# Performance work log

Hardware: AMD Instinct MI355X
Metric: run time of the kernel (lower is better)

Reference implementation:

```python
import jax, jax.numpy as jnp
import numpy as np

D_MODEL = 1024
NUM_HEADS = 16
HEAD_DIM = D_MODEL // NUM_HEADS
BATCH, SEQ = 2, 2048


def setup_inputs() -> dict:
    key = jax.random.key(0)
    ks = jax.random.split(key, 11)
    s = 1.0 / np.sqrt(D_MODEL)
    inp = {
        "query": jax.random.normal(ks[0], (BATCH, SEQ, D_MODEL), jnp.float32),
        "key": jax.random.normal(ks[1], (BATCH, SEQ, D_MODEL), jnp.float32),
        "value": jax.random.normal(ks[2], (BATCH, SEQ, D_MODEL), jnp.float32),
        "q_w": jax.random.uniform(ks[3], (D_MODEL, D_MODEL), jnp.float32, -s, s),
        "q_b": jax.random.uniform(ks[4], (D_MODEL,), jnp.float32, -s, s),
        "k_w": jax.random.uniform(ks[5], (D_MODEL, D_MODEL), jnp.float32, -s, s),
        "k_b": jax.random.uniform(ks[6], (D_MODEL,), jnp.float32, -s, s),
        "v_w": jax.random.uniform(ks[7], (D_MODEL, D_MODEL), jnp.float32, -s, s),
        "v_b": jax.random.uniform(ks[8], (D_MODEL,), jnp.float32, -s, s),
        "o_w": jax.random.uniform(ks[9], (D_MODEL, D_MODEL), jnp.float32, -s, s),
        "o_b": jax.random.uniform(ks[10], (D_MODEL,), jnp.float32, -s, s),
    }
    return inp


def reference(query, key, value, q_w, q_b, k_w, k_b, v_w, v_b, o_w, o_b):
    B = query.shape[0]
    # linear projections (torch Linear: x @ W^T + b)
    q = query @ q_w.T + q_b
    k = key @ k_w.T + k_b
    v = value @ v_w.T + v_b
    # split heads: [B, S, D] -> [B, H, S, Hd]
    def split(x):
        return x.reshape(B, -1, NUM_HEADS, HEAD_DIM).transpose(0, 2, 1, 3)
    q, k, v = split(q), split(k), split(v)
    scores = jnp.einsum("bhqd,bhkd->bhqk", q, k) / np.sqrt(HEAD_DIM).astype(np.float32)
    attn = jax.nn.softmax(scores, axis=-1)
    out = jnp.einsum("bhqk,bhkd->bhqd", attn, v)  # [B,H,S,Hd]
    merged = out.transpose(0, 2, 1, 3).reshape(B, -1, D_MODEL)
    return merged @ o_w.T + o_b
```

## Files before the change

### kernel.cpp

```cpp
#include <hip/hip_runtime.h>
#include <hip/hip_bf16.h>

typedef unsigned short u16;
typedef unsigned int u32;
typedef __attribute__((ext_vector_type(8))) short short8;
typedef __attribute__((ext_vector_type(4))) short s16x4;
typedef __attribute__((ext_vector_type(4))) float f32x4;
typedef __attribute__((ext_vector_type(4))) u32 u32v4;

__device__ __forceinline__ u16 f2bf(float f) {
    u32 u = __float_as_uint(f);
    return (u16)((u + 0x7FFFu + ((u >> 16) & 1u)) >> 16);
}
__device__ __forceinline__ u32 pack2bf(float a, float b) {
    __hip_bfloat162 h = __float22bfloat162_rn(float2{a, b});
    return *reinterpret_cast<u32*>(&h);
}
__device__ __forceinline__ float exp2hw(float x) {
    float r;
    asm("v_exp_f32 %0, %1" : "=v"(r) : "v"(x));
    return r;
}

__device__ __forceinline__ void gload16(const void* g, void* s) {
    __builtin_amdgcn_global_load_lds(
        (const __attribute__((address_space(1))) void*)g,
        (__attribute__((address_space(3))) void*)s, 16, 0, 0);
}

__global__ __launch_bounds__(256) void cast_all_kernel(
    const float* __restrict__ s0, const float* __restrict__ s1, const float* __restrict__ s2,
    const float* __restrict__ s3, const float* __restrict__ s4, const float* __restrict__ s5,
    const float* __restrict__ s6,
    u16* __restrict__ d0, u16* __restrict__ d1, u16* __restrict__ d2,
    u16* __restrict__ d3, u16* __restrict__ d4, u16* __restrict__ d5,
    u16* __restrict__ d6, int nBig, int nSmall)
{
    const int y = blockIdx.y;
    const float* s = y == 0 ? s0 : (y == 1 ? s1 : (y == 2 ? s2 : (y == 3 ? s3 : (y == 4 ? s4 : (y == 5 ? s5 : s6)))));
    u16* d = y == 0 ? d0 : (y == 1 ? d1 : (y == 2 ? d2 : (y == 3 ? d3 : (y == 4 ? d4 : (y == 5 ? d5 : d6)))));
    const int n = (y < 3) ? nBig : nSmall;
    int i = (blockIdx.x * 256 + threadIdx.x) * 4;
    const int stride = gridDim.x * 256 * 4;
    for (; i < n; i += stride) {
        float4 v = *(const float4*)(s + i);
        uint2 t;
        t.x = pack2bf(v.x, v.y);
        t.y = pack2bf(v.z, v.w);
        *(uint2*)(d + i) = t;
    }
}

__global__ __launch_bounds__(256) void qkv_gemm(
    const u16* __restrict__ Xq, const u16* __restrict__ Xk, const u16* __restrict__ Xv,
    const u16* __restrict__ Wqkv,
    const float* __restrict__ qb, const float* __restrict__ kb, const float* __restrict__ vb,
    u16* __restrict__ Qo, u16* __restrict__ Ko, u16* __restrict__ Vo)
{
    constexpr int K = 1024;
    __shared__ __align__(16) u16 Asm[2][4096];
    __shared__ __align__(16) u16 Bsm[2][4096];

    const int tid = threadIdx.x;
    const int wid = tid >> 6;
    const int lane = tid & 63;
    const int r15 = lane & 15, g = lane >> 4;
    const int flat = blockIdx.x;
    const int wgid = (flat & 7) * 96 + (flat >> 3);
    const int m0 = (wgid / 24) * 128;
    const int nAll = (wgid % 24) * 128;
    const int z = nAll >> 10;
    const u16* A = z == 0 ? Xq : (z == 1 ? Xk : Xv);
    const int wr = wid >> 1, wc = wid & 1;

    f32x4 acc[4][4];
#pragma unroll
    for (int i = 0; i < 4; ++i)
#pragma unroll
        for (int j = 0; j < 4; ++j) acc[i][j] = (f32x4){0.f, 0.f, 0.f, 0.f};

    const int idx0 = tid, idx1 = tid + 256;
    const size_t aoff0 = (size_t)(m0 + (idx0 >> 2)) * K + (idx0 & 3) * 8;
    const size_t aoff1 = (size_t)(m0 + (idx1 >> 2)) * K + (idx1 & 3) * 8;
    const size_t boff0 = (size_t)(nAll + (idx0 >> 2)) * K + (idx0 & 3) * 8;
    const size_t boff1 = (size_t)(nAll + (idx1 >> 2)) * K + (idx1 & 3) * 8;
    const u16* abase = &Asm[0][0] + (wr * 64 + r15) * 32 + g * 8;
    const u16* bbase = &Bsm[0][0] + (wc * 64 + r15) * 32 + g * 8;

    gload16(A + aoff0, &Asm[0][wid * 512]);
    gload16(A + aoff1, &Asm[0][2048 + wid * 512]);
    gload16(Wqkv + boff0, &Bsm[0][wid * 512]);
    gload16(Wqkv + boff1, &Bsm[0][2048 + wid * 512]);
    __syncthreads();

#pragma unroll 2
    for (int t = 0; t < 32; ++t) {
        const int buf = t & 1;
        if (t < 31) {
            const int kt = (t + 1) * 32;
            gload16(A + aoff0 + kt, &Asm[buf ^ 1][wid * 512]);
            gload16(A + aoff1 + kt, &Asm[buf ^ 1][2048 + wid * 512]);
            gload16(Wqkv + boff0 + kt, &Bsm[buf ^ 1][wid * 512]);
            gload16(Wqkv + boff1 + kt, &Bsm[buf ^ 1][2048 + wid * 512]);
        }
        short8 af[4], bfr[4];
#pragma unroll
        for (int i = 0; i < 4; ++i) {
            af[i]  = *(const short8*)(abase + buf * 4096 + i * 512);
            bfr[i] = *(const short8*)(bbase + buf * 4096 + i * 512);
        }
#pragma unroll
        for (int i = 0; i < 4; ++i)
#pragma unroll
            for (int j = 0; j < 4; ++j)
                acc[i][j] = __builtin_amdgcn_mfma_f32_16x16x32_bf16(af[i], bfr[j], acc[i][j], 0, 0, 0);
        __syncthreads();
    }

    const float scale = (z == 0) ? 0.125f * 1.4426950408889634f : 1.0f;
    u16* ob = z == 0 ? Qo : (z == 1 ? Ko : Vo);
    const float* bias = z == 0 ? qb : (z == 1 ? kb : vb);
    const int nloc0 = nAll & 1023;
#pragma unroll
    for (int i = 0; i < 4; ++i) {
        const int mbase = m0 + wr * 64 + i * 16 + g * 4;
#pragma unroll
        for (int j = 0; j < 4; ++j) {
            const int n = nloc0 + wc * 64 + j * 16 + r15;
            const float bb = bias[n];
            if (z < 2) {
#pragma unroll
                for (int r = 0; r < 4; ++r)
                    ob[(size_t)(mbase + r) * 1024 + n] = f2bf((acc[i][j][r] + bb) * scale);
            } else {
                const int b_ = mbase >> 11, s_ = mbase & 2047;
                const int blk = (s_ >> 2) & 7;
                const int pb = ((blk & 3) << 1) | (blk >> 2);
                const int s_new = (s_ & ~31) | (pb << 2);
                s16x4 pk;
#pragma unroll
                for (int r = 0; r < 4; ++r) pk[r] = (short)f2bf(acc[i][j][r] + bb);
                *(s16x4*)(ob + ((size_t)b_ << 21) + (size_t)n * 2048 + s_new) = pk;
            }
        }
    }
}

__global__ __launch_bounds__(256) void o_gemm(
    const u16* __restrict__ A, const u16* __restrict__ W,
    const float* __restrict__ bias, float* __restrict__ outp)
{
    constexpr int N = 1024, K = 1024;
    __shared__ __align__(16) u16 Asm[2][4096];
    __shared__ __align__(16) u16 Bsm[2][4096];
    const int tid = threadIdx.x;
    const int wid = tid >> 6;
    const int lane = tid & 63;
    const int r15 = lane & 15, g = lane >> 4;
    const int fb = blockIdx.y * 8 + blockIdx.x;
    const int lsw = (fb & 7) * 32 + (fb >> 3);
    const int m0 = (lsw >> 3) * 128, n0 = (lsw & 7) * 128;
    const int wr = wid >> 1, wc = wid & 1;

    f32x4 acc[4][4];
#pragma unroll
    for (int i = 0; i < 4; ++i)
#pragma unroll
        for (int j = 0; j < 4; ++j) acc[i][j] = (f32x4){0.f, 0.f, 0.f, 0.f};

    const int idx0 = tid, idx1 = tid + 256;
    const size_t aoff0 = (size_t)(m0 + (idx0 >> 2)) * K + (idx0 & 3) * 8;
    const size_t aoff1 = (size_t)(m0 + (idx1 >> 2)) * K + (idx1 & 3) * 8;
    const size_t boff0 = (size_t)(n0 + (idx0 >> 2)) * K + (idx0 & 3) * 8;
    const size_t boff1 = (size_t)(n0 + (idx1 >> 2)) * K + (idx1 & 3) * 8;
    const u16* abase = &Asm[0][0] + (wr * 64 + r15) * 32 + g * 8;
    const u16* bbase = &Bsm[0][0] + (wc * 64 + r15) * 32 + g * 8;

    gload16(A + aoff0, &Asm[0][wid * 512]);
    gload16(A + aoff1, &Asm[0][2048 + wid * 512]);
    gload16(W + boff0, &Bsm[0][wid * 512]);
    gload16(W + boff1, &Bsm[0][2048 + wid * 512]);
    __syncthreads();

#pragma unroll 2
    for (int t = 0; t < 32; ++t) {
        const int buf = t & 1;
        if (t < 31) {
            const int kt = (t + 1) * 32;
            gload16(A + aoff0 + kt, &Asm[buf ^ 1][wid * 512]);
            gload16(A + aoff1 + kt, &Asm[buf ^ 1][2048 + wid * 512]);
            gload16(W + boff0 + kt, &Bsm[buf ^ 1][wid * 512]);
            gload16(W + boff1 + kt, &Bsm[buf ^ 1][2048 + wid * 512]);
        }
        short8 af[4], bfr[4];
#pragma unroll
        for (int i = 0; i < 4; ++i) {
            af[i]  = *(const short8*)(abase + buf * 4096 + i * 512);
            bfr[i] = *(const short8*)(bbase + buf * 4096 + i * 512);
        }
#pragma unroll
        for (int i = 0; i < 4; ++i)
#pragma unroll
            for (int j = 0; j < 4; ++j)
                acc[i][j] = __builtin_amdgcn_mfma_f32_16x16x32_bf16(af[i], bfr[j], acc[i][j], 0, 0, 0);
        __syncthreads();
    }

#pragma unroll
    for (int i = 0; i < 4; ++i) {
        const int mbase = m0 + wr * 64 + i * 16 + g * 4;
#pragma unroll
        for (int j = 0; j < 4; ++j) {
            const int n = n0 + wc * 64 + j * 16 + r15;
            const float bb = bias[n];
#pragma unroll
            for (int r = 0; r < 4; ++r)
                outp[(size_t)(mbase + r) * N + n] = acc[i][j][r] + bb;
        }
    }
}

__global__ __launch_bounds__(256) void attn_kernel(
    const u16* __restrict__ Q, const u16* __restrict__ Kb,
    const u16* __restrict__ Vt, u16* __restrict__ Mo)
{
    __shared__ __align__(16) u16 Ksm[2][4096];
    __shared__ __align__(16) u16 Vsm[2][4096];
    const int tid = threadIdx.x;
    const int wid = tid >> 6, lane = tid & 63;
    const int r15 = lane & 15, g = lane >> 4;
    const int bid = blockIdx.x;
    const int l = (bid & 7) * 64 + (bid >> 3);
    const int bh = l >> 4;
    const int b = bh >> 4, h = bh & 15;
    const int q0 = (l & 15) * 128 + wid * 32;

    const u16* Qbase = Q + ((size_t)b * 2048 + q0) * 1024 + h * 64;
    short8 qf[2][2];
#pragma unroll
    for (int qt = 0; qt < 2; ++qt)
#pragma unroll
        for (int f = 0; f < 2; ++f)
            qf[qt][f] = *(const short8*)(Qbase + (size_t)(qt * 16 + r15) * 1024 + f * 32 + g * 8);

    const int p0 = tid, p1 = tid + 256;
    const int row0 = p0 >> 3, slot0s = (p0 & 7) ^ (row0 & 7);
    const int row1 = p1 >> 3, slot1s = (p1 & 7) ^ (row1 & 7);
    const u16* Ks0 = Kb + ((size_t)b * 2048 + row0) * 1024 + h * 64 + slot0s * 8;
    const u16* Ks1 = Kb + ((size_t)b * 2048 + row1) * 1024 + h * 64 + slot1s * 8;
    const u16* Vs0 = Vt + ((size_t)b << 21) + (size_t)(h * 64 + row0) * 2048 + slot0s * 8;
    const u16* Vs1 = Vt + ((size_t)b << 21) + (size_t)(h * 64 + row1) * 2048 + slot1s * 8;

    const int sA = r15 & 7;
    const int sl0 = (g ^ sA) * 8;
    const int sl1 = sl0 ^ 32;
    const u16* kb0 = &Ksm[0][0] + r15 * 64 + sl0;
    const u16* kb1 = &Ksm[0][0] + r15 * 64 + sl1;
    const u16* vb0 = &Vsm[0][0] + r15 * 64 + sl0;
    const u16* vb1 = &Vsm[0][0] + r15 * 64 + sl1;

    f32x4 acc[2][4];
#pragma unroll
    for (int qt = 0; qt < 2; ++qt)
#pragma unroll
        for (int d4 = 0; d4 < 4; ++d4) acc[qt][d4] = (f32x4){0.f, 0.f, 0.f, 0.f};
    f32x4 accl[2] = {(f32x4){0.f, 0.f, 0.f, 0.f}, (f32x4){0.f, 0.f, 0.f, 0.f}};
    const short8 vone = {0x3F80, 0x3F80, 0x3F80, 0x3F80, 0x3F80, 0x3F80, 0x3F80, 0x3F80};

    gload16(Ks0, &Ksm[0][wid * 512]);
    gload16(Ks1, &Ksm[0][2048 + wid * 512]);
    gload16(Vs0, &Vsm[0][wid * 512]);
    gload16(Vs1, &Vsm[0][2048 + wid * 512]);
    Ks0 += 65536; Ks1 += 65536; Vs0 += 64; Vs1 += 64;
    __syncthreads();

#pragma unroll 2
    for (int t = 0; t < 32; ++t) {
        const int buf = t & 1;
        if (t < 31) {
            gload16(Ks0, &Ksm[buf ^ 1][wid * 512]);
            gload16(Ks1, &Ksm[buf ^ 1][2048 + wid * 512]);
            gload16(Vs0, &Vsm[buf ^ 1][wid * 512]);
            gload16(Vs1, &Vsm[buf ^ 1][2048 + wid * 512]);
            Ks0 += 65536; Ks1 += 65536; Vs0 += 64; Vs1 += 64;
        }

        short8 kf[4][2];
#pragma unroll
        for (int kt = 0; kt < 4; ++kt) {
            kf[kt][0] = *(const short8*)(kb0 + buf * 4096 + kt * 1024);
            kf[kt][1] = *(const short8*)(kb1 + buf * 4096 + kt * 1024);
        }

        f32x4 st[2][4];
#pragma unroll
        for (int qt = 0; qt < 2; ++qt)
#pragma unroll
            for (int kt = 0; kt < 4; ++kt) {
                f32x4 zz = (f32x4){0.f, 0.f, 0.f, 0.f};
                zz = __builtin_amdgcn_mfma_f32_16x16x32_bf16(kf[kt][0], qf[qt][0], zz, 0, 0, 0);
                zz = __builtin_amdgcn_mfma_f32_16x16x32_bf16(kf[kt][1], qf[qt][1], zz, 0, 0, 0);
                st[qt][kt] = zz;
            }

        u32v4 pA[2], pB[2];
#pragma unroll
        for (int qt = 0; qt < 2; ++qt) {
#pragma unroll
            for (int kt = 0; kt < 4; ++kt) {
                float e0 = exp2hw(st[qt][kt][0]);
                float e1 = exp2hw(st[qt][kt][1]);
                float e2 = exp2hw(st[qt][kt][2]);
                float e3 = exp2hw(st[qt][kt][3]);
                u32 lo = pack2bf(e0, e1);
                u32 hi = pack2bf(e2, e3);
                if (kt < 2) { pA[qt][kt * 2] = lo; pA[qt][kt * 2 + 1] = hi; }
                else        { pB[qt][(kt - 2) * 2] = lo; pB[qt][(kt - 2) * 2 + 1] = hi; }
            }
        }

        accl[0] = __builtin_amdgcn_mfma_f32_16x16x32_bf16(vone, __builtin_bit_cast(short8, pA[0]), accl[0], 0, 0, 0);
        accl[0] = __builtin_amdgcn_mfma_f32_16x16x32_bf16(vone, __builtin_bit_cast(short8, pB[0]), accl[0], 0, 0, 0);
        accl[1] = __builtin_amdgcn_mfma_f32_16x16x32_bf16(vone, __builtin_bit_cast(short8, pA[1]), accl[1], 0, 0, 0);
        accl[1] = __builtin_amdgcn_mfma_f32_16x16x32_bf16(vone, __builtin_bit_cast(short8, pB[1]), accl[1], 0, 0, 0);

#pragma unroll
        for (int d4 = 0; d4 < 4; ++d4) {
            short8 vf0 = *(const short8*)(vb0 + buf * 4096 + d4 * 1024);
            short8 vf1 = *(const short8*)(vb1 + buf * 4096 + d4 * 1024);
            acc[0][d4] = __builtin_amdgcn_mfma_f32_16x16x32_bf16(vf0, __builtin_bit_cast(short8, pA[0]), acc[0][d4], 0, 0, 0);
            acc[0][d4] = __builtin_amdgcn_mfma_f32_16x16x32_bf16(vf1, __builtin_bit_cast(short8, pB[0]), acc[0][d4], 0, 0, 0);
            acc[1][d4] = __builtin_amdgcn_mfma_f32_16x16x32_bf16(vf0, __builtin_bit_cast(short8, pA[1]), acc[1][d4], 0, 0, 0);
            acc[1][d4] = __builtin_amdgcn_mfma_f32_16x16x32_bf16(vf1, __builtin_bit_cast(short8, pB[1]), acc[1][d4], 0, 0, 0);
        }
        __syncthreads();
    }

#pragma unroll
    for (int qt = 0; qt < 2; ++qt) {
        const float inv = 1.f / accl[qt][0];
        const size_t orow = ((size_t)b * 2048 + q0 + qt * 16 + r15) * 1024 + h * 64;
#pragma unroll
        for (int d4 = 0; d4 < 4; ++d4) {
            uint2 o;
            o.x = pack2bf(acc[qt][d4][0] * inv, acc[qt][d4][1] * inv);
            o.y = pack2bf(acc[qt][d4][2] * inv, acc[qt][d4][3] * inv);
            *(uint2*)(Mo + orow + d4 * 16 + g * 4) = o;
        }
    }
}

extern "C" void kernel_launch(void* const* d_in, const int* in_sizes, int n_in,
                              void* d_out, int out_size, void* d_ws, size_t ws_size,
                              hipStream_t stream) {
    (void)in_sizes; (void)n_in; (void)out_size; (void)ws_size;
    const float* query = (const float*)d_in[0];
    const float* key   = (const float*)d_in[1];
    const float* value = (const float*)d_in[2];
    const float* q_w = (const float*)d_in[3];
    const float* q_b = (const float*)d_in[4];
    const float* k_w = (const float*)d_in[5];
    const float* k_b = (const float*)d_in[6];
    const float* v_w = (const float*)d_in[7];
    const float* v_b = (const float*)d_in[8];
    const float* o_w = (const float*)d_in[9];
    const float* o_b = (const float*)d_in[10];

    const size_t NE = (size_t)4096 * 1024;
    const size_t MW = (size_t)1024 * 1024;
    u16* w = (u16*)d_ws;
    u16* Xq = w;
    u16* Xk = Xq + NE;
    u16* Xv = Xk + NE;
    u16* Wq = Xv + NE;
    u16* Wk = Wq + MW;
    u16* Wv = Wk + MW;
    u16* Wo = Wv + MW;
    u16* Qb = Wo + MW;
    u16* Kb = Qb + NE;
    u16* Vt = Kb + NE;
    u16* Mo = Vt + NE;

    cast_all_kernel<<<dim3(2048, 7), 256, 0, stream>>>(
        query, key, value, q_w, k_w, v_w, o_w,
        Xq, Xk, Xv, Wq, Wk, Wv, Wo, (int)NE, (int)MW);
    qkv_gemm<<<dim3(768), 256, 0, stream>>>(
        Xq, Xk, Xv, Wq, q_b, k_b, v_b, Qb, Kb, Vt);
    attn_kernel<<<dim3(512), 256, 0, stream>>>(Qb, Kb, Vt, Mo);
    o_gemm<<<dim3(8, 32), 256, 0, stream>>>(Mo, Wo, o_b, (float*)d_out);
}
```

Baseline: 143.0 us.

## Use partial vmcnt waits to keep next-tile loads in flight across barriers

```diff
diff --git a/kernel.cpp b/kernel.cpp
--- a/kernel.cpp
+++ b/kernel.cpp
@@ -27,6 +27,11 @@
         (const __attribute__((address_space(1))) void*)g,
         (__attribute__((address_space(3))) void*)s, 16, 0, 0);
 }
+
+#define VM4()  asm volatile("s_waitcnt vmcnt(4)" ::: "memory")
+#define VM0()  asm volatile("s_waitcnt vmcnt(0)" ::: "memory")
+#define BAR()  __builtin_amdgcn_s_barrier()
+#define SCB()  __builtin_amdgcn_sched_barrier(0)
 
 __global__ __launch_bounds__(256) void cast_all_kernel(
     const float* __restrict__ s0, const float* __restrict__ s1, const float* __restrict__ s2,
@@ -66,10 +71,11 @@
     const int lane = tid & 63;
     const int r15 = lane & 15, g = lane >> 4;
     const int flat = blockIdx.x;
-    const int wgid = (flat & 7) * 96 + (flat >> 3);
-    const int m0 = (wgid / 24) * 128;
-    const int nAll = (wgid % 24) * 128;
-    const int z = nAll >> 10;
+    const int z = flat >> 8;
+    const int fb = flat & 255;
+    const int lsw = (fb & 7) * 32 + (fb >> 3);
+    const int m0 = (lsw >> 3) * 128, n0 = (lsw & 7) * 128;
+    const int nAll = (z << 10) + n0;
     const u16* A = z == 0 ? Xq : (z == 1 ? Xk : Xv);
     const int wr = wid >> 1, wc = wid & 1;
 
@@ -87,22 +93,20 @@
     const u16* abase = &Asm[0][0] + (wr * 64 + r15) * 32 + g * 8;
     const u16* bbase = &Bsm[0][0] + (wc * 64 + r15) * 32 + g * 8;
 
-    gload16(A + aoff0, &Asm[0][wid * 512]);
-    gload16(A + aoff1, &Asm[0][2048 + wid * 512]);
-    gload16(Wqkv + boff0, &Bsm[0][wid * 512]);
-    gload16(Wqkv + boff1, &Bsm[0][2048 + wid * 512]);
-    __syncthreads();
-
+    auto STAGE = [&](int buf, int kt) {
+        gload16(A + aoff0 + kt, &Asm[buf][wid * 512]);
+        gload16(A + aoff1 + kt, &Asm[buf][2048 + wid * 512]);
+        gload16(Wqkv + boff0 + kt, &Bsm[buf][wid * 512]);
+        gload16(Wqkv + boff1 + kt, &Bsm[buf][2048 + wid * 512]);
+    };
+
+    STAGE(0, 0);
 #pragma unroll 2
     for (int t = 0; t < 32; ++t) {
         const int buf = t & 1;
-        if (t < 31) {
-            const int kt = (t + 1) * 32;
-            gload16(A + aoff0 + kt, &Asm[buf ^ 1][wid * 512]);
-            gload16(A + aoff1 + kt, &Asm[buf ^ 1][2048 + wid * 512]);
-            gload16(Wqkv + boff0 + kt, &Bsm[buf ^ 1][wid * 512]);
-            gload16(Wqkv + boff1 + kt, &Bsm[buf ^ 1][2048 + wid * 512]);
-        }
+        if (t < 31) { STAGE(buf ^ 1, (t + 1) * 32); VM4(); }
+        else        { VM0(); }
+        BAR(); SCB();
         short8 af[4], bfr[4];
 #pragma unroll
         for (int i = 0; i < 4; ++i) {
@@ -114,19 +118,18 @@
 #pragma unroll
             for (int j = 0; j < 4; ++j)
                 acc[i][j] = __builtin_amdgcn_mfma_f32_16x16x32_bf16(af[i], bfr[j], acc[i][j], 0, 0, 0);
-        __syncthreads();
+        BAR();
     }
 
     const float scale = (z == 0) ? 0.125f * 1.4426950408889634f : 1.0f;
     u16* ob = z == 0 ? Qo : (z == 1 ? Ko : Vo);
     const float* bias = z == 0 ? qb : (z == 1 ? kb : vb);
-    const int nloc0 = nAll & 1023;
 #pragma unroll
     for (int i = 0; i < 4; ++i) {
         const int mbase = m0 + wr * 64 + i * 16 + g * 4;
 #pragma unroll
         for (int j = 0; j < 4; ++j) {
-            const int n = nloc0 + wc * 64 + j * 16 + r15;
+            const int n = n0 + wc * 64 + j * 16 + r15;
             const float bb = bias[n];
             if (z < 2) {
 #pragma unroll
@@ -176,22 +179,20 @@
     const u16* abase = &Asm[0][0] + (wr * 64 + r15) * 32 + g * 8;
     const u16* bbase = &Bsm[0][0] + (wc * 64 + r15) * 32 + g * 8;
 
-    gload16(A + aoff0, &Asm[0][wid * 512]);
-    gload16(A + aoff1, &Asm[0][2048 + wid * 512]);
-    gload16(W + boff0, &Bsm[0][wid * 512]);
-    gload16(W + boff1, &Bsm[0][2048 + wid * 512]);
-    __syncthreads();
-
+    auto STAGE = [&](int buf, int kt) {
+        gload16(A + aoff0 + kt, &Asm[buf][wid * 512]);
+        gload16(A + aoff1 + kt, &Asm[buf][2048 + wid * 512]);
+        gload16(W + boff0 + kt, &Bsm[buf][wid * 512]);
+        gload16(W + boff1 + kt, &Bsm[buf][2048 + wid * 512]);
+    };
+
+    STAGE(0, 0);
 #pragma unroll 2
     for (int t = 0; t < 32; ++t) {
         const int buf = t & 1;
-        if (t < 31) {
-            const int kt = (t + 1) * 32;
-            gload16(A + aoff0 + kt, &Asm[buf ^ 1][wid * 512]);
-            gload16(A + aoff1 + kt, &Asm[buf ^ 1][2048 + wid * 512]);
-            gload16(W + boff0 + kt, &Bsm[buf ^ 1][wid * 512]);
-            gload16(W + boff1 + kt, &Bsm[buf ^ 1][2048 + wid * 512]);
-        }
+        if (t < 31) { STAGE(buf ^ 1, (t + 1) * 32); VM4(); }
+        else        { VM0(); }
+        BAR(); SCB();
         short8 af[4], bfr[4];
 #pragma unroll
         for (int i = 0; i < 4; ++i) {
@@ -203,7 +204,7 @@
 #pragma unroll
             for (int j = 0; j < 4; ++j)
                 acc[i][j] = __builtin_amdgcn_mfma_f32_16x16x32_bf16(af[i], bfr[j], acc[i][j], 0, 0, 0);
-        __syncthreads();
+        BAR();
     }
 
 #pragma unroll
@@ -267,23 +268,21 @@
     f32x4 accl[2] = {(f32x4){0.f, 0.f, 0.f, 0.f}, (f32x4){0.f, 0.f, 0.f, 0.f}};
     const short8 vone = {0x3F80, 0x3F80, 0x3F80, 0x3F80, 0x3F80, 0x3F80, 0x3F80, 0x3F80};
 
-    gload16(Ks0, &Ksm[0][wid * 512]);
-    gload16(Ks1, &Ksm[0][2048 + wid * 512]);
-    gload16(Vs0, &Vsm[0][wid * 512]);
-    gload16(Vs1, &Vsm[0][2048 + wid * 512]);
-    Ks0 += 65536; Ks1 += 65536; Vs0 += 64; Vs1 += 64;
-    __syncthreads();
-
+    auto STAGE = [&](int buf) {
+        gload16(Ks0, &Ksm[buf][wid * 512]);
+        gload16(Ks1, &Ksm[buf][2048 + wid * 512]);
+        gload16(Vs0, &Vsm[buf][wid * 512]);
+        gload16(Vs1, &Vsm[buf][2048 + wid * 512]);
+        Ks0 += 65536; Ks1 += 65536; Vs0 += 64; Vs1 += 64;
+    };
+
+    STAGE(0);
 #pragma unroll 2
     for (int t = 0; t < 32; ++t) {
         const int buf = t & 1;
-        if (t < 31) {
-            gload16(Ks0, &Ksm[buf ^ 1][wid * 512]);
-            gload16(Ks1, &Ksm[buf ^ 1][2048 + wid * 512]);
-            gload16(Vs0, &Vsm[buf ^ 1][wid * 512]);
-            gload16(Vs1, &Vsm[buf ^ 1][2048 + wid * 512]);
-            Ks0 += 65536; Ks1 += 65536; Vs0 += 64; Vs1 += 64;
-        }
+        if (t < 31) { STAGE(buf ^ 1); VM4(); }
+        else        { VM0(); }
+        BAR(); SCB();
 
         short8 kf[4][2];
 #pragma unroll
@@ -333,7 +332,7 @@
             acc[1][d4] = __builtin_amdgcn_mfma_f32_16x16x32_bf16(vf0, __builtin_bit_cast(short8, pA[1]), acc[1][d4], 0, 0, 0);
             acc[1][d4] = __builtin_amdgcn_mfma_f32_16x16x32_bf16(vf1, __builtin_bit_cast(short8, pB[1]), acc[1][d4], 0, 0, 0);
         }
-        __syncthreads();
+        BAR();
     }
 
 #pragma unroll
```

After: 141.4 us, median of 2. Within noise of the previous version (-1.1%).
